# Performance work log

Measured on AMD Instinct MI355X. Metric: run time of the kernel, lower is better.

Reference implementation:

```python
import jax, jax.numpy as jnp
import numpy as np

EMBED_DIM = 768

def setup_inputs() -> dict:
    key = jax.random.key(0)
    ks = jax.random.split(key, 5)
    C = EMBED_DIM
    x = jax.random.normal(ks[0], (32, 1024, C), dtype=jnp.float32)
    s = 1.0 / np.sqrt(C)
    W_qkv = jax.random.normal(ks[1], (C, 3 * C), dtype=jnp.float32) * s
    b_qkv = jnp.zeros((3 * C,), dtype=jnp.float32)
    W_proj = jax.random.normal(ks[2], (C, C), dtype=jnp.float32) * s
    b_proj = jnp.zeros((C,), dtype=jnp.float32)
    return {"x": x, "W_qkv": W_qkv, "b_qkv": b_qkv, "W_proj": W_proj, "b_proj": b_proj}

def reference(x, W_qkv, b_qkv, W_proj, b_proj):
    B, N, C = x.shape
    qkv = x @ W_qkv + b_qkv                      # [B, N, 3C]
    q, k, v = jnp.split(qkv, 3, axis=-1)         # each [B, N, C]
    scale = 1.0 / jnp.sqrt(jnp.asarray(C, dtype=x.dtype))
    attn = jnp.einsum('bnc,bmc->bnm', q, k) * scale  # [B, N, N]
    attn = jax.nn.softmax(attn, axis=-1)
    out = jnp.einsum('bnm,bmc->bnc', attn, v)    # [B, N, C]
    return out @ W_proj + b_proj
```

## Files before the change

kernel.cpp:

```cpp
#include <hip/hip_runtime.h>

typedef __bf16 bf16;
typedef __bf16 bf16x4 __attribute__((ext_vector_type(4)));
typedef __bf16 bf16x8 __attribute__((ext_vector_type(8)));
typedef float f32x4 __attribute__((ext_vector_type(4)));

constexpr int BATCH = 32;
constexpr int SEQ   = 1024;
constexpr int CDIM  = 768;
constexpr int ROWS  = BATCH * SEQ;
constexpr int QKVC  = 3 * CDIM;

constexpr size_t oWqT = 0;
constexpr size_t oWpT = oWqT + (size_t)QKVC * CDIM * 2;
constexpr size_t oQKV = oWpT + (size_t)CDIM * CDIM * 2;
constexpr size_t oS   = oQKV + (size_t)ROWS * QKVC * 2;
constexpr size_t oVT  = oS   + (size_t)BATCH * SEQ * SEQ * 2;
constexpr size_t oInv = oVT  + (size_t)BATCH * CDIM * SEQ * 2;
constexpr size_t oAO  = oQKV;
constexpr size_t oXB  = oS;
constexpr size_t oPart= oWqT;

__device__ __forceinline__ void gld_lds16(const void* g, void* l) {
  __builtin_amdgcn_global_load_lds(
      (const __attribute__((address_space(1))) unsigned int*)g,
      (__attribute__((address_space(3))) unsigned int*)l,
      16, 0, 0);
}

__global__ __launch_bounds__(256) void f2b_kernel(const float* __restrict__ x,
                                                  bf16* __restrict__ y) {
  int i = blockIdx.x * blockDim.x + threadIdx.x;
  const float* p = x + (size_t)i * 8;
  float4 a = *(const float4*)p;
  float4 b = *(const float4*)(p + 4);
  bf16x8 o;
  o[0]=(bf16)a.x; o[1]=(bf16)a.y; o[2]=(bf16)a.z; o[3]=(bf16)a.w;
  o[4]=(bf16)b.x; o[5]=(bf16)b.y; o[6]=(bf16)b.z; o[7]=(bf16)b.w;
  *(bf16x8*)(y + (size_t)i * 8) = o;
}

__global__ __launch_bounds__(256) void wt_kernel(const float* __restrict__ W,
                                                 bf16* __restrict__ T, int N) {
  __shared__ float t[32][33];
  int k0 = blockIdx.x * 32, n0 = blockIdx.y * 32;
  int tx = threadIdx.x & 31, ty = threadIdx.x >> 5;
  #pragma unroll
  for (int i = 0; i < 4; ++i)
    t[ty + i * 8][tx] = W[(size_t)(k0 + ty + i * 8) * N + n0 + tx];
  __syncthreads();
  #pragma unroll
  for (int i = 0; i < 4; ++i)
    T[(size_t)(n0 + ty + i * 8) * 768 + k0 + tx] = (bf16)t[tx][ty + i * 8];
}

__global__ __launch_bounds__(256) void finish_kernel(const float* __restrict__ partial,
                                                     float* __restrict__ inv) {
  int i = blockIdx.x * 256 + threadIdx.x;
  float4 p = *(const float4*)(partial + (size_t)i * 4);
  inv[i] = 1.0f / (p.x + p.y + p.z + p.w);
}


#define LOADA(mh_) do {                                                          \
  _Pragma("unroll")                                                              \
  for (int i_ = 0; i_ < 4; ++i_) {                                               \
    const int row_ = wm * 128 + ((mh_) * 4 + i_) * 16 + lr;                      \
    const char* rb_ = (const char*)Acur + row_ * 128;                            \
    af[i_][0] = *(const bf16x8*)(rb_ + ((0  + kb0) ^ swz));                      \
    af[i_][1] = *(const bf16x8*)(rb_ + ((64 + kb0) ^ swz));                      \
  }                                                                              \
} while (0)

#define STAGE2(sp0_, sp1_) do {                                                  \
  if (t + 1 < nkt) {                                                             \
    gld_lds16(Ast + (size_t)((sp0_) * 64) * lda + ktn, Asn + (sp0_) * 4096 + wv * 512); \
    gld_lds16(Bst + (size_t)((sp0_) * 64) * ldb + ktn, Bsn + (sp0_) * 4096 + wv * 512); \
    gld_lds16(Ast + (size_t)((sp1_) * 64) * lda + ktn, Asn + (sp1_) * 4096 + wv * 512); \
    gld_lds16(Bst + (size_t)((sp1_) * 64) * ldb + ktn, Bsn + (sp1_) * 4096 + wv * 512); \
  }                                                                              \
} while (0)

#define PHASE(mh_, nh_, LA_, STG_) do {                                          \
  if (LA_) LOADA(mh_);                                                           \
  bf16x8 bfr[2][2];                                                              \
  _Pragma("unroll")                                                              \
  for (int j_ = 0; j_ < 2; ++j_) {                                               \
    const int row_ = wn * 64 + ((nh_) * 2 + j_) * 16 + lr;                       \
    const char* rb_ = (const char*)Bcur + row_ * 128;                            \
    bfr[j_][0] = *(const bf16x8*)(rb_ + ((0  + kb0) ^ swz));                     \
    bfr[j_][1] = *(const bf16x8*)(rb_ + ((64 + kb0) ^ swz));                     \
  }                                                                              \
  STG_;                                                                          \
  asm volatile("s_waitcnt lgkmcnt(0)" ::: "memory");                             \
  __builtin_amdgcn_sched_barrier(0);                                             \
  __builtin_amdgcn_s_setprio(1);                                                 \
  _Pragma("unroll")                                                              \
  for (int ks_ = 0; ks_ < 2; ++ks_)                                              \
    _Pragma("unroll")                                                            \
    for (int i_ = 0; i_ < 4; ++i_)                                               \
      _Pragma("unroll")                                                          \
      for (int j_ = 0; j_ < 2; ++j_)                                             \
        acc[(mh_) * 4 + i_][(nh_) * 2 + j_] =                                    \
            __builtin_amdgcn_mfma_f32_16x16x32_bf16(af[i_][ks_], bfr[j_][ks_],   \
                acc[(mh_) * 4 + i_][(nh_) * 2 + j_], 0, 0, 0);                   \
  __builtin_amdgcn_s_setprio(0);                                                 \
} while (0)

template<bool OUT_BF16, bool HAS_BIAS, bool ROW_SCALE, bool FUSE_EXP, bool TR_V>
__global__ __launch_bounds__(512, 2) void gemm256(
    const bf16* __restrict__ Ap, const bf16* __restrict__ Bp, void* __restrict__ Cp,
    int K, int lda, int ldb, int ldc, int ntm, int ntn,
    long sA, long sB, long sC,
    float scale, const float* __restrict__ rowScale, long sRS,
    const float* __restrict__ bias, float* __restrict__ partial,
    bf16* __restrict__ vtout)
{
  __shared__ __align__(16) bf16 LDSB[4][256 * 64];
  const int tid  = threadIdx.x;
  const int lane = tid & 63;
  const int wv   = tid >> 6;
  const int wm   = wv >> 2;
  const int wn   = wv & 3;

  const int total = (int)gridDim.x;
  const int chunk = total >> 3;
  const int bid   = (int)blockIdx.x;
  int sbid = (bid & 7) * chunk + (bid >> 3);
  const int pb = ntm * ntn;
  const int z  = sbid / pb;  sbid -= z * pb;
  const int mt = sbid / ntn;
  const int nt = sbid - mt * ntn;
  const int m0 = mt * 256, n0 = nt * 256;

  const bf16* A = Ap + (size_t)z * sA;
  const bf16* B = Bp + (size_t)z * sB;

  const int sr  = tid >> 3;
  const int sc8 = tid & 7;
  const int gch = sc8 ^ (sr & 7);
  const bf16* Ast = A + (size_t)(m0 + sr) * lda + gch * 8;
  const bf16* Bst = B + (size_t)(n0 + sr) * ldb + gch * 8;

  const int lr  = lane & 15;
  const int swz = (lane & 7) << 4;
  const int kb0 = (lane >> 4) * 16;

  f32x4 acc[8][4] = {};

  #pragma unroll
  for (int p = 0; p < 4; ++p) {
    gld_lds16(Ast + (size_t)(p * 64) * lda, &LDSB[0][p * 4096 + wv * 512]);
    gld_lds16(Bst + (size_t)(p * 64) * ldb, &LDSB[2][p * 4096 + wv * 512]);
  }
  asm volatile("s_waitcnt vmcnt(0)" ::: "memory");
  __builtin_amdgcn_s_barrier();
  __builtin_amdgcn_sched_barrier(0);

  const int nkt = K >> 6;
  for (int t = 0; t < nkt; ++t) {
    const int cur = t & 1;
    const bf16* Acur = LDSB[cur];
    const bf16* Bcur = LDSB[2 + cur];
    bf16* Asn = LDSB[cur ^ 1];
    bf16* Bsn = LDSB[2 + (cur ^ 1)];
    const int ktn = (t + 1) << 6;
    bf16x8 af[4][2];
    PHASE(0, 0, 1, STAGE2(0, 1));
    PHASE(0, 1, 0, STAGE2(2, 3));
    PHASE(1, 1, 1, ;);
    PHASE(1, 0, 0, ;);
    asm volatile("s_waitcnt vmcnt(0)" ::: "memory");
    __builtin_amdgcn_s_barrier();
    __builtin_amdgcn_sched_barrier(0);
  }

  if (TR_V && nt >= 6) {
    bf16* tile = LDSB[0];
    __syncthreads();
    #pragma unroll
    for (int mf = 0; mf < 8; ++mf) {
      #pragma unroll
      for (int nf = 0; nf < 4; ++nf) {
        const int lm = wm * 128 + mf * 16 + (lane >> 4) * 4;
        const int lc = wn * 64 + nf * 16 + (lane & 15);
        bf16x4 w;
        #pragma unroll
        for (int r = 0; r < 4; ++r) {
          float v = acc[mf][nf][r] * scale;
          if (HAS_BIAS) v += bias[n0 + lc];
          w[r] = (bf16)v;
        }
        *(bf16x4*)((char*)tile + lc * 512 + ((lm * 2) ^ ((lc & 7) << 4))) = w;
      }
    }
    __syncthreads();
    const int bz = m0 >> 10;
    const int mb = m0 & 1023;
    bf16* dst = vtout + ((size_t)bz * CDIM + (n0 - 2 * CDIM)) * SEQ + mb;
    #pragma unroll
    for (int it = 0; it < 16; ++it) {
      const int c  = (tid >> 5) + it * 16;
      const int ch = tid & 31;
      bf16x8 vv = *(const bf16x8*)((const char*)tile + c * 512 + ((ch * 16) ^ ((c & 7) << 4)));
      *(bf16x8*)(dst + (size_t)c * SEQ + ch * 8) = vv;
    }
  } else if (FUSE_EXP) {
    float rs[8][4];
    #pragma unroll
    for (int mf = 0; mf < 8; ++mf)
      #pragma unroll
      for (int r = 0; r < 4; ++r) rs[mf][r] = 0.f;
    #pragma unroll
    for (int mf = 0; mf < 8; ++mf)
      #pragma unroll
      for (int nf = 0; nf < 4; ++nf)
        #pragma unroll
        for (int r = 0; r < 4; ++r) {
          int gm = m0 + wm * 128 + mf * 16 + ((lane >> 4) * 4 + r);
          int gn = n0 + wn * 64 + nf * 16 + (lane & 15);
          float e = __expf(acc[mf][nf][r] * scale);
          ((bf16*)Cp)[(size_t)z * sC + (size_t)gm * ldc + gn] = (bf16)e;
          rs[mf][r] += e;
        }
    float* sl = (float*)LDSB;
    #pragma unroll
    for (int mf = 0; mf < 8; ++mf)
      #pragma unroll
      for (int r = 0; r < 4; ++r) {
        float s = rs[mf][r];
        s += __shfl_xor(s, 1); s += __shfl_xor(s, 2);
        s += __shfl_xor(s, 4); s += __shfl_xor(s, 8);
        if ((lane & 15) == 0)
          sl[wn * 256 + wm * 128 + mf * 16 + (lane >> 4) * 4 + r] = s;
      }
    __syncthreads();
    if (tid < 256) {
      float s = sl[tid] + sl[256 + tid] + sl[512 + tid] + sl[768 + tid];
      partial[((size_t)z * SEQ + m0 + tid) * 4 + nt] = s;
    }
  } else {
    #pragma unroll
    for (int mf = 0; mf < 8; ++mf) {
      #pragma unroll
      for (int nf = 0; nf < 4; ++nf) {
        #pragma unroll
        for (int r = 0; r < 4; ++r) {
          int gm = m0 + wm * 128 + mf * 16 + ((lane >> 4) * 4 + r);
          int gn = n0 + wn * 64 + nf * 16 + (lane & 15);
          float v = acc[mf][nf][r] * scale;
          if (ROW_SCALE) v *= rowScale[(size_t)z * sRS + gm];
          if (HAS_BIAS)  v += bias[gn];
          if (OUT_BF16) ((bf16*)Cp)[(size_t)z * sC + (size_t)gm * ldc + gn] = (bf16)v;
          else          ((float*)Cp)[(size_t)z * sC + (size_t)gm * ldc + gn] = v;
        }
      }
    }
  }
}

extern "C" void kernel_launch(void* const* d_in, const int* in_sizes, int n_in,
                              void* d_out, int out_size, void* d_ws, size_t ws_size,
                              hipStream_t stream) {
  const float* x     = (const float*)d_in[0];
  const float* Wqkv  = (const float*)d_in[1];
  const float* bqkv  = (const float*)d_in[2];
  const float* Wproj = (const float*)d_in[3];
  const float* bproj = (const float*)d_in[4];
  float* out = (float*)d_out;
  char*  ws  = (char*)d_ws;

  bf16*  WqT = (bf16*)(ws + oWqT);
  bf16*  WpT = (bf16*)(ws + oWpT);
  bf16*  qkv = (bf16*)(ws + oQKV);
  bf16*  S   = (bf16*)(ws + oS);
  bf16*  VT  = (bf16*)(ws + oVT);
  float* inv = (float*)(ws + oInv);
  bf16*  AO  = (bf16*)(ws + oAO);
  bf16*  xb  = (bf16*)(ws + oXB);
  float* part= (float*)(ws + oPart);

  const float qk_scale = 1.0f / sqrtf((float)CDIM);

  f2b_kernel<<<ROWS * CDIM / 8 / 256, 256, 0, stream>>>(x, xb);
  wt_kernel<<<dim3(768 / 32, QKVC / 32), 256, 0, stream>>>(Wqkv, WqT, QKVC);
  wt_kernel<<<dim3(768 / 32, CDIM / 32), 256, 0, stream>>>(Wproj, WpT, CDIM);

  gemm256<true, true, false, false, true><<<(ROWS / 256) * (QKVC / 256), 512, 0, stream>>>(
      xb, WqT, qkv, CDIM, CDIM, CDIM, QKVC, ROWS / 256, QKVC / 256,
      0, 0, 0, 1.0f, nullptr, 0, bqkv, nullptr, VT);

  gemm256<true, false, false, true, false><<<BATCH * (SEQ / 256) * (SEQ / 256), 512, 0, stream>>>(
      qkv, qkv + CDIM, S, CDIM, QKVC, QKVC, SEQ, SEQ / 256, SEQ / 256,
      (long)SEQ * QKVC, (long)SEQ * QKVC, (long)SEQ * SEQ, qk_scale, nullptr, 0, nullptr, part, nullptr);

  finish_kernel<<<ROWS / 256, 256, 0, stream>>>(part, inv);

  gemm256<true, false, true, false, false><<<BATCH * (SEQ / 256) * (CDIM / 256), 512, 0, stream>>>(
      S, VT, AO, SEQ, SEQ, SEQ, CDIM, SEQ / 256, CDIM / 256,
      (long)SEQ * SEQ, (long)CDIM * SEQ, (long)SEQ * CDIM, 1.0f, inv, SEQ, nullptr, nullptr, nullptr);

  gemm256<false, true, false, false, false><<<(ROWS / 256) * (CDIM / 256), 512, 0, stream>>>(
      AO, WpT, out, CDIM, CDIM, CDIM, CDIM, ROWS / 256, CDIM / 256,
      0, 0, 0, 1.0f, nullptr, 0, bproj, nullptr, nullptr);
}
```

Before: 358.2 us.

## Restructure GEMM main loop into 8-wave ping-pong with staggered A/B prefetch

```diff
diff --git a/kernel.cpp b/kernel.cpp
--- a/kernel.cpp
+++ b/kernel.cpp
@@ -62,36 +62,41 @@
 }
 
 
-#define LOADA(mh_) do {                                                          \
+#define DSRD_A(dst_, qm_) do {                                                   \
   _Pragma("unroll")                                                              \
   for (int i_ = 0; i_ < 4; ++i_) {                                               \
-    const int row_ = wm * 128 + ((mh_) * 4 + i_) * 16 + lr;                      \
+    const int row_ = wm * 128 + (qm_) * 64 + i_ * 16 + lr;                       \
     const char* rb_ = (const char*)Acur + row_ * 128;                            \
-    af[i_][0] = *(const bf16x8*)(rb_ + ((0  + kb0) ^ swz));                      \
-    af[i_][1] = *(const bf16x8*)(rb_ + ((64 + kb0) ^ swz));                      \
+    dst_[i_][0] = *(const bf16x8*)(rb_ + ((0  + kb0) ^ swz));                    \
+    dst_[i_][1] = *(const bf16x8*)(rb_ + ((64 + kb0) ^ swz));                    \
   }                                                                              \
 } while (0)
 
-#define STAGE2(sp0_, sp1_) do {                                                  \
-  if (t + 1 < nkt) {                                                             \
-    gld_lds16(Ast + (size_t)((sp0_) * 64) * lda + ktn, Asn + (sp0_) * 4096 + wv * 512); \
-    gld_lds16(Bst + (size_t)((sp0_) * 64) * ldb + ktn, Bsn + (sp0_) * 4096 + wv * 512); \
-    gld_lds16(Ast + (size_t)((sp1_) * 64) * lda + ktn, Asn + (sp1_) * 4096 + wv * 512); \
-    gld_lds16(Bst + (size_t)((sp1_) * 64) * ldb + ktn, Bsn + (sp1_) * 4096 + wv * 512); \
-  }                                                                              \
-} while (0)
-
-#define PHASE(mh_, nh_, LA_, STG_) do {                                          \
-  if (LA_) LOADA(mh_);                                                           \
-  bf16x8 bfr[2][2];                                                              \
+#define DSRD_B(dst_, qn_) do {                                                   \
   _Pragma("unroll")                                                              \
   for (int j_ = 0; j_ < 2; ++j_) {                                               \
-    const int row_ = wn * 64 + ((nh_) * 2 + j_) * 16 + lr;                       \
+    const int row_ = wn * 64 + (qn_) * 32 + j_ * 16 + lr;                        \
     const char* rb_ = (const char*)Bcur + row_ * 128;                            \
-    bfr[j_][0] = *(const bf16x8*)(rb_ + ((0  + kb0) ^ swz));                     \
-    bfr[j_][1] = *(const bf16x8*)(rb_ + ((64 + kb0) ^ swz));                     \
+    dst_[j_][0] = *(const bf16x8*)(rb_ + ((0  + kb0) ^ swz));                    \
+    dst_[j_][1] = *(const bf16x8*)(rb_ + ((64 + kb0) ^ swz));                    \
   }                                                                              \
-  STG_;                                                                          \
+} while (0)
+
+#define STG_A(buf_, kt_, h_) do {                                                \
+  gld_lds16(Ast + (size_t)((h_) * 128 +  0) * lda + (size_t)(kt_) * 64,          \
+            &LDSB[(buf_)][((h_) * 2 + 0) * 4096 + wv * 512]);                    \
+  gld_lds16(Ast + (size_t)((h_) * 128 + 64) * lda + (size_t)(kt_) * 64,          \
+            &LDSB[(buf_)][((h_) * 2 + 1) * 4096 + wv * 512]);                    \
+} while (0)
+
+#define STG_B(buf_, kt_, h_) do {                                                \
+  gld_lds16(Bst + (size_t)((h_) * 128 +  0) * ldb + (size_t)(kt_) * 64,          \
+            &LDSB[2 + (buf_)][((h_) * 2 + 0) * 4096 + wv * 512]);                \
+  gld_lds16(Bst + (size_t)((h_) * 128 + 64) * ldb + (size_t)(kt_) * 64,          \
+            &LDSB[2 + (buf_)][((h_) * 2 + 1) * 4096 + wv * 512]);                \
+} while (0)
+
+#define MMA16(a_, b_, mo_, no_) do {                                             \
   asm volatile("s_waitcnt lgkmcnt(0)" ::: "memory");                             \
   __builtin_amdgcn_sched_barrier(0);                                             \
   __builtin_amdgcn_s_setprio(1);                                                 \
@@ -101,11 +106,14 @@
     for (int i_ = 0; i_ < 4; ++i_)                                               \
       _Pragma("unroll")                                                          \
       for (int j_ = 0; j_ < 2; ++j_)                                             \
-        acc[(mh_) * 4 + i_][(nh_) * 2 + j_] =                                    \
-            __builtin_amdgcn_mfma_f32_16x16x32_bf16(af[i_][ks_], bfr[j_][ks_],   \
-                acc[(mh_) * 4 + i_][(nh_) * 2 + j_], 0, 0, 0);                   \
+        acc[(mo_) + i_][(no_) + j_] =                                            \
+            __builtin_amdgcn_mfma_f32_16x16x32_bf16(a_[i_][ks_], b_[j_][ks_],    \
+                acc[(mo_) + i_][(no_) + j_], 0, 0, 0);                           \
   __builtin_amdgcn_s_setprio(0);                                                 \
 } while (0)
+
+#define PIN() __builtin_amdgcn_sched_barrier(0)
+#define BAR() __builtin_amdgcn_s_barrier()
 
 template<bool OUT_BF16, bool HAS_BIAS, bool ROW_SCALE, bool FUSE_EXP, bool TR_V>
 __global__ __launch_bounds__(512, 2) void gemm256(
@@ -147,32 +155,50 @@
   const int kb0 = (lane >> 4) * 16;
 
   f32x4 acc[8][4] = {};
-
-  #pragma unroll
-  for (int p = 0; p < 4; ++p) {
-    gld_lds16(Ast + (size_t)(p * 64) * lda, &LDSB[0][p * 4096 + wv * 512]);
-    gld_lds16(Bst + (size_t)(p * 64) * ldb, &LDSB[2][p * 4096 + wv * 512]);
+  const int nkt = K >> 6;
+
+  STG_A(0, 0, 0); STG_A(0, 0, 1);
+  STG_B(0, 0, 0); STG_B(0, 0, 1);
+  if (nkt > 1) {
+    STG_A(1, 1, 0); STG_A(1, 1, 1);
+    asm volatile("s_waitcnt vmcnt(4)" ::: "memory");
+  } else {
+    asm volatile("s_waitcnt vmcnt(0)" ::: "memory");
   }
-  asm volatile("s_waitcnt vmcnt(0)" ::: "memory");
-  __builtin_amdgcn_s_barrier();
-  __builtin_amdgcn_sched_barrier(0);
-
-  const int nkt = K >> 6;
+  BAR(); PIN();
+
+  bf16x8 a0[4][2], a1[4][2], b0[2][2], b1[2][2];
   for (int t = 0; t < nkt; ++t) {
     const int cur = t & 1;
     const bf16* Acur = LDSB[cur];
     const bf16* Bcur = LDSB[2 + cur];
-    bf16* Asn = LDSB[cur ^ 1];
-    bf16* Bsn = LDSB[2 + (cur ^ 1)];
-    const int ktn = (t + 1) << 6;
-    bf16x8 af[4][2];
-    PHASE(0, 0, 1, STAGE2(0, 1));
-    PHASE(0, 1, 0, STAGE2(2, 3));
-    PHASE(1, 1, 1, ;);
-    PHASE(1, 0, 0, ;);
-    asm volatile("s_waitcnt vmcnt(0)" ::: "memory");
-    __builtin_amdgcn_s_barrier();
-    __builtin_amdgcn_sched_barrier(0);
+    const bool sb = (t + 1 < nkt), sa = (t + 2 < nkt);
+    DSRD_A(a0, 0); DSRD_B(b0, 0);
+    PIN();
+    if (sb) STG_B(cur ^ 1, t + 1, 0);
+    BAR();
+    MMA16(a0, b0, 0, 0);
+    BAR();
+    DSRD_A(a1, 1);
+    PIN();
+    if (sb) STG_B(cur ^ 1, t + 1, 1);
+    BAR();
+    MMA16(a1, b0, 4, 0);
+    BAR();
+    DSRD_B(b1, 1);
+    PIN();
+    if (sa) STG_A(cur, t + 2, 0);
+    BAR();
+    MMA16(a1, b1, 4, 2);
+    BAR();
+    PIN();
+    if (sa) STG_A(cur, t + 2, 1);
+    BAR();
+    MMA16(a0, b1, 0, 2);
+    if (sa) asm volatile("s_waitcnt vmcnt(4)" ::: "memory");
+    else    asm volatile("s_waitcnt vmcnt(0)" ::: "memory");
+    BAR();
+    PIN();
   }
 
   if (TR_V && nt >= 6) {
@@ -224,6 +250,7 @@
           rs[mf][r] += e;
         }
     float* sl = (float*)LDSB;
+    __syncthreads();
     #pragma unroll
     for (int mf = 0; mf < 8; ++mf)
       #pragma unroll
```

Result: no change. 364.9 us (+1.9%).
